# Optimization experiments

Hardware: AMD Instinct MI355X
Metric: run time of the kernel (lower is better)

The kernel has to match this reference:

```python
import jax, jax.numpy as jnp
import numpy as np

B, C_IN, C_OUT, H, W = 8, 512, 512, 64, 64
KS = 3
STYLE_DIM = 512
UP = 2            # AliasFreeConv passes upsample*2 = 2 to the activation
DOWN = 2
TAPS = 12
MARGIN = 10
NEG_SLOPE = 0.2
LRELU_SCALE = float(np.sqrt(2.0))  # fused_leaky_relu default scale
EPS = 1e-8


def _lowpass(taps):
    # 1D windowed-sinc lowpass (separable FIR), normalized to sum 1
    n = np.arange(taps)
    x = n - (taps - 1) / 2.0
    h = np.sinc(x / 2.0) * np.hanning(taps)
    return (h / h.sum()).astype(np.float32)


def upfirdn2d(x, kernel, up, down, pad):
    # x: (N,C,H,W); kernel: (kh,kw); up=(ux,uy); down=(dx,dy); pad=(px0,px1,py0,py1)
    # Semantics match rosinality upfirdn2d_native: zero-stuff, pad, convolve with
    # flipped kernel, stride-downsample. lhs_dilation gives (L-1)*u+1 samples, the
    # torch version keeps L*u (u-1 trailing zeros), so add u-1 to trailing pad.
    ux, uy = up
    dx, dy = down
    px0, px1, py0, py1 = pad
    N, C, H_, W_ = x.shape
    k = jnp.flip(kernel, axis=(0, 1))[None, None].astype(x.dtype)  # (1,1,kh,kw)
    y = x.reshape(N * C, 1, H_, W_)
    y = jax.lax.conv_general_dilated(
        y, k, window_strides=(dy, dx),
        padding=((py0, py1 + uy - 1), (px0, px1 + ux - 1)),
        lhs_dilation=(uy, ux),
        dimension_numbers=('NCHW', 'OIHW', 'NCHW'))
    return y.reshape(N, C, y.shape[2], y.shape[3])


def setup_inputs() -> dict:
    key = jax.random.key(0)
    ks = jax.random.split(key, 6)
    x = jax.random.normal(ks[0], (B, C_IN, H, W), jnp.float32)
    style = jax.random.normal(ks[1], (B, STYLE_DIM), jnp.float32)
    mod_w = jax.random.normal(ks[2], (C_IN, STYLE_DIM), jnp.float32)   # EqualLinear weight
    mod_b = jnp.ones((C_IN,), jnp.float32)                              # bias_init=1
    conv_w = jax.random.normal(ks[3], (C_OUT, C_IN, KS, KS), jnp.float32)
    act_b = jax.random.normal(ks[4], (C_OUT,), jnp.float32) * 0.1
    lp = jnp.asarray(_lowpass(TAPS))
    return {"x": x, "style": style, "mod_w": mod_w, "mod_b": mod_b,
            "conv_w": conv_w, "act_b": act_b, "up_filter": lp, "down_filter": lp}


def reference(x, style, mod_w, mod_b, conv_w, act_b, up_filter, down_filter):
    Bn, Cin, _, _ = x.shape
    # --- ModulatedConv2d (padding=False, eval mode: ema_var = 1) ---
    lin_scale = 1.0 / np.sqrt(STYLE_DIM)          # EqualLinear scale, lr_mul=1
    s = style @ (mod_w * lin_scale).T + mod_b     # (B, Cin)
    wscale = 1.0 / np.sqrt(Cin * KS * KS)
    w = wscale * conv_w[None] * s[:, None, :, None, None]  # (B, Cout, Cin, kh, kw)
    demod = jax.lax.rsqrt(jnp.sum(w * w, axis=(2, 3, 4)) + EPS)
    w = w * demod[:, :, None, None, None]
    w = w / (1.0 + EPS)                           # / (sqrt(ema_var)+eps), ema_var=1

    def conv_one(xi, wi):  # per-sample grouped conv (groups=batch), VALID padding
        return jax.lax.conv_general_dilated(
            xi[None], wi, (1, 1), 'VALID',
            dimension_numbers=('NCHW', 'OIHW', 'NCHW'))[0]
    out = jax.vmap(conv_one)(x, w)                # (B, Cout, H-2, W-2)

    # --- AliasFreeActivation ---
    out = out + act_b[None, :, None, None]
    fu = up_filter * UP                           # 1D filter scaled by upsample at init
    p = TAPS - UP
    up_pad = ((p + 1) // 2 + UP * 2 - 1, p // 2 + UP)  # padding flag False (ks==3)
    out = upfirdn2d(out, fu[None, :], up=(UP, 1), down=(1, 1),
                    pad=(up_pad[0], up_pad[1], 0, 0))
    out = upfirdn2d(out, fu[:, None], up=(1, UP), down=(1, 1),
                    pad=(0, 0, up_pad[0], up_pad[1]))
    out = jnp.where(out >= 0, out, NEG_SLOPE * out) * LRELU_SCALE
    p = TAPS - DOWN
    dpad = ((p + 1) // 2, p // 2)
    out = upfirdn2d(out, down_filter[None, :], up=(1, 1), down=(DOWN, 1),
                    pad=(dpad[0], dpad[1], 0, 0))
    out = upfirdn2d(out, down_filter[:, None], up=(1, 1), down=(1, DOWN),
                    pad=(0, 0, dpad[0], dpad[1]))
    m = (MARGIN * UP - MARGIN * DOWN) // 2        # = 0 here (static)
    if m > 0:
        out = out[:, :, m:-m, m:-m]
    return out
```

## Files before the change

### kernel.cpp

```cpp
#include <hip/hip_runtime.h>

typedef __attribute__((ext_vector_type(8))) short s16x8;
typedef __attribute__((ext_vector_type(4))) float f32x4;

__device__ __forceinline__ float b2f(unsigned short u){
  union { unsigned int i; float f; } v; v.i = ((unsigned int)u) << 16; return v.f;
}
__device__ __forceinline__ unsigned short f2b(float f){
  union { float f; unsigned int i; } v; v.f = f;
  unsigned int x = v.i;
  return (unsigned short)((x + 0x7fffu + ((x >> 16) & 1u)) >> 16);
}

__device__ __forceinline__ void ld_lds16(const unsigned short* g, unsigned short* l){
  __builtin_amdgcn_global_load_lds(
      (const __attribute__((address_space(1))) void*)g,
      (__attribute__((address_space(3))) void*)l, 16, 0, 0);
}

template<int BF16> struct In;
template<> struct In<1>{
  static __device__ __forceinline__ float ld(const void* p, size_t i){
    return b2f(((const unsigned short*)p)[i]);
  }
};
template<> struct In<0>{
  static __device__ __forceinline__ float ld(const void* p, size_t i){
    return ((const float*)p)[i];
  }
};

__global__ void k_detect(const unsigned int* __restrict__ mod_b, int* __restrict__ flag){
  *flag = (*mod_b == 0x3F803F80u) ? 1 : 0;
}

template<int BF16>
__device__ __forceinline__ void small_body(const void* actb, const void* upf, const void* dnf,
                                           float* actb_f, float* fu_f, float* fd_f){
  int t = threadIdx.x;
  actb_f[t] = In<BF16>::ld(actb, t);
  if(t < 12){
    fu_f[t] = 2.0f * In<BF16>::ld(upf, t);
    fd_f[t] = In<BF16>::ld(dnf, t);
  }
}
__global__ void k_small(const void* __restrict__ actb, const void* __restrict__ upf,
                        const void* __restrict__ dnf, float* __restrict__ actb_f,
                        float* __restrict__ fu_f, float* __restrict__ fd_f,
                        const int* __restrict__ flag){
  if(*flag) small_body<1>(actb, upf, dnf, actb_f, fu_f, fd_f);
  else      small_body<0>(actb, upf, dnf, actb_f, fu_f, fd_f);
}

template<int BF16>
__device__ __forceinline__ void style_body(const void* style, const void* mod_w,
                                           const void* mod_b, float* s){
  int gw = (blockIdx.x*256 + threadIdx.x) >> 6;
  int lane = threadIdx.x & 63;
  int b = gw >> 9, i = gw & 511;
  size_t so = (size_t)b*512 + lane*8;
  size_t mo = (size_t)i*512 + lane*8;
  float acc = 0.f;
  #pragma unroll
  for(int q=0;q<8;q++) acc += In<BF16>::ld(style, so+q)*In<BF16>::ld(mod_w, mo+q);
  #pragma unroll
  for(int m=32;m>=1;m>>=1) acc += __shfl_xor(acc, m, 64);
  if(lane == 0) s[gw] = acc * 0.044194173824159216f + In<BF16>::ld(mod_b, i);
}
__global__ __launch_bounds__(256) void k_style(
    const void* __restrict__ style, const void* __restrict__ mod_w,
    const void* __restrict__ mod_b, float* __restrict__ s,
    const int* __restrict__ flag){
  if(*flag) style_body<1>(style, mod_w, mod_b, s);
  else      style_body<0>(style, mod_w, mod_b, s);
}

template<int BF16>
__device__ __forceinline__ void wrepq_body(const void* conv_w, unsigned short* wrep2, float* wsq){
  int idx = blockIdx.x*256 + threadIdx.x;
  float v[9], acc = 0.f;
  #pragma unroll
  for(int t=0;t<9;t++){ v[t] = In<BF16>::ld(conv_w, (size_t)idx*9 + t); acc += v[t]*v[t]; }
  wsq[idx] = acc;
  #pragma unroll
  for(int t=0;t<9;t++) wrep2[t*262144 + idx] = f2b(v[t]);
}
__global__ __launch_bounds__(256) void k_wrepq(
    const void* __restrict__ conv_w, unsigned short* __restrict__ wrep2,
    float* __restrict__ wsq, const int* __restrict__ flag){
  if(*flag) wrepq_body<1>(conv_w, wrep2, wsq);
  else      wrepq_body<0>(conv_w, wrep2, wsq);
}

__global__ __launch_bounds__(256) void k_demod(
    const float* __restrict__ s, const float* __restrict__ wsq,
    float* __restrict__ rowscale){
  int gw = (blockIdx.x*256 + threadIdx.x) >> 6;
  int lane = threadIdx.x & 63;
  int b = gw >> 9, o = gw & 511;
  const float* sr = s + b*512 + lane*8;
  const float* wr = wsq + (size_t)o*512 + lane*8;
  float acc = 0.f;
  #pragma unroll
  for(int q=0;q<8;q++){ float sv = sr[q]; acc += sv*sv*wr[q]; }
  #pragma unroll
  for(int m=32;m>=1;m>>=1) acc += __shfl_xor(acc, m, 64);
  if(lane == 0){
    float demod = rsqrtf(acc*(1.0f/4608.0f) + 1e-8f);
    rowscale[gw] = 0.014731391274719742f * demod * (1.0f/(1.0f+1e-8f));
  }
}

template<int BF16>
__device__ __forceinline__ void xs_body(const void* x, const float* s,
                                        unsigned short* xs2, unsigned short* tl){
  int bh = blockIdx.x >> 3;
  int i0 = (blockIdx.x & 7) << 6;
  int b = bh >> 6, h = bh & 63;
  #pragma unroll
  for(int l=0;l<2;l++){
    int e = (threadIdx.x + l*256) << 3;
    int row = e >> 6, col = e & 63;
    size_t base = (((size_t)(b*512 + i0 + row))*64 + h)*64 + col;
    float sc = s[b*512 + i0 + row];
    alignas(16) unsigned short tmp[8];
    if(BF16){
      uint4 v = *(const uint4*)((const unsigned short*)x + base);
      const unsigned short* pv = (const unsigned short*)&v;
      #pragma unroll
      for(int q2=0;q2<8;q2++) tmp[q2] = f2b(b2f(pv[q2]) * sc);
    } else {
      float4 v0 = *(const float4*)((const float*)x + base);
      float4 v1 = *(const float4*)((const float*)x + base + 4);
      tmp[0]=f2b(v0.x*sc); tmp[1]=f2b(v0.y*sc); tmp[2]=f2b(v0.z*sc); tmp[3]=f2b(v0.w*sc);
      tmp[4]=f2b(v1.x*sc); tmp[5]=f2b(v1.y*sc); tmp[6]=f2b(v1.z*sc); tmp[7]=f2b(v1.w*sc);
    }
    *(uint4*)(tl + row*72 + col) = *(const uint4*)tmp;
  }
  __syncthreads();
  #pragma unroll
  for(int l=0;l<2;l++){
    int e = (threadIdx.x + l*256) << 3;
    int w = e >> 6, ic = e & 63;
    alignas(16) unsigned short tmp[8];
    #pragma unroll
    for(int q2=0;q2<8;q2++) tmp[q2] = tl[(ic + q2)*72 + w];
    *(uint4*)(xs2 + (((size_t)(b*64 + h))*64 + w)*512 + i0 + ic) = *(const uint4*)tmp;
  }
}
__global__ __launch_bounds__(256) void k_xs(
    const void* __restrict__ x, const float* __restrict__ s,
    unsigned short* __restrict__ xs2, const int* __restrict__ flag){
  __shared__ unsigned short tl[64*72];
  if(*flag) xs_body<1>(x, s, xs2, tl);
  else      xs_body<0>(x, s, xs2, tl);
}


#define MFMA16(a,b,c) __builtin_amdgcn_mfma_f32_16x16x32_bf16((a),(b),(c),0,0,0)
#define KBARRIER __builtin_amdgcn_s_barrier()
#define LGKM0 asm volatile("s_waitcnt lgkmcnt(0)" ::: "memory")
#define LGKM8 asm volatile("s_waitcnt lgkmcnt(8)" ::: "memory")
#define VMW4  asm volatile("s_waitcnt vmcnt(4)" ::: "memory")
#define VMW8  asm volatile("s_waitcnt vmcnt(8)" ::: "memory")
#define VMW0  asm volatile("s_waitcnt vmcnt(0)" ::: "memory")

template<int MH,int NH>
__device__ __forceinline__ void mmq(f32x4 (&acc)[8][4], const s16x8 (&Ax)[8], const s16x8 (&Bx)[4]){
  #pragma unroll
  for(int j=0;j<4;j++)
    #pragma unroll
    for(int k=0;k<2;k++){
      f32x4 c = acc[MH*4+j][NH*2+k];
      c = MFMA16(Ax[j*2+0], Bx[k*2+0], c);
      c = MFMA16(Ax[j*2+1], Bx[k*2+1], c);
      acc[MH*4+j][NH*2+k] = c;
    }
}

template<int BUF,int MH>
__device__ __forceinline__ void lda(s16x8 (&dst)[8], const unsigned short* lds,
                                    int arow, int c0, int c1){
  #pragma unroll
  for(int j=0;j<4;j++){
    const unsigned short* p = lds + BUF*32768 + arow + (MH*64 + j*16)*64;
    dst[j*2+0] = *(const s16x8*)(p + c0);
    dst[j*2+1] = *(const s16x8*)(p + c1);
  }
}

template<int BUF,int NH>
__device__ __forceinline__ void ldb(s16x8 (&dst)[4], const unsigned short* lds,
                                    int brow, int c0, int c1){
  #pragma unroll
  for(int k=0;k<2;k++){
    const unsigned short* p = lds + BUF*32768 + brow + (NH*2 + k)*16*64;
    dst[k*2+0] = *(const s16x8*)(p + c0);
    dst[k*2+1] = *(const s16x8*)(p + c1);
  }
}

template<int BUF,int H>
__device__ __forceinline__ void stga(const unsigned short* wrep2, unsigned short* lds,
                                     const unsigned (&aoff)[2][2], int sdst, int kt){
  unsigned koff = (unsigned)(kt >> 3)*262144u + (unsigned)(kt & 7)*64u;
  ld_lds16(wrep2 + aoff[H][0] + koff, lds + BUF*32768 + H*8192 + 0*4096 + sdst);
  ld_lds16(wrep2 + aoff[H][1] + koff, lds + BUF*32768 + H*8192 + 1*4096 + sdst);
}

template<int BUF,int H>
__device__ __forceinline__ void stgb(const unsigned short* xs2, unsigned short* lds,
                                     const unsigned (&boff)[2][2], int sdst, int kt){
  int t = kt >> 3;
  int kh = (t*11) >> 5;
  unsigned koff = (unsigned)(kh*64 + (t - kh*3))*512u + (unsigned)(kt & 7)*64u;
  ld_lds16(xs2 + boff[H][0] + koff, lds + BUF*32768 + 16384 + H*8192 + 0*4096 + sdst);
  ld_lds16(xs2 + boff[H][1] + koff, lds + BUF*32768 + 16384 + H*8192 + 1*4096 + sdst);
}

__global__ __launch_bounds__(512, 2) void k_conv(
    const unsigned short* __restrict__ wrep2,
    const unsigned short* __restrict__ xs2,
    const float* __restrict__ rowscale,
    const float* __restrict__ actb_f,
    unsigned short* __restrict__ out0){
  __shared__ unsigned short lds[65536];

  const int tid  = threadIdx.x;
  const int lane = tid & 63, wid = tid >> 6;
  const int wm = wid >> 2, wn = wid & 3;
  const int quad = lane >> 4, l16 = lane & 15, sw = l16 & 7;

  int w = blockIdx.x;
  int wsw = (w & 7)*31 + (w >> 3);
  const int mt = wsw & 1, nt = wsw >> 1;
  const int o0 = mt*256, p0 = nt*256;

  const int srow  = tid >> 3;
  const int sgoff = ((tid & 7) ^ (srow & 7)) * 8;
  unsigned aoff[2][2], boff[2][2];
  #pragma unroll
  for(int h=0;h<2;h++){
    #pragma unroll
    for(int r=0;r<2;r++){
      int row = srow + r*64 + h*128;
      aoff[h][r] = (unsigned)(o0 + row)*512u + (unsigned)sgoff;
      int p  = p0 + row;
      int bb = ((p >> 7)*529) >> 14;
      boff[h][r] = (unsigned)(p + bb*128)*512u + (unsigned)sgoff;
    }
  }
  const int sdst = wid*512;

  const int c0 = ((0*4 + quad) ^ sw) * 8;
  const int c1 = ((1*4 + quad) ^ sw) * 8;
  const int arow = (wm*128 + l16) * 64;
  const int brow = (wn*64  + l16) * 64 + 16384;

  f32x4 acc[8][4];
  f32x4 z = {0.f,0.f,0.f,0.f};
  #pragma unroll
  for(int a=0;a<8;a++)
    #pragma unroll
    for(int n=0;n<4;n++) acc[a][n] = z;

  s16x8 Aa[8], Ab[8], Ba[4], Bb[4];

  stga<0,0>(wrep2, lds, aoff, sdst, 0);
  stga<0,1>(wrep2, lds, aoff, sdst, 0);
  stgb<0,0>(xs2,   lds, boff, sdst, 0);
  stgb<0,1>(xs2,   lds, boff, sdst, 0);
  stga<1,0>(wrep2, lds, aoff, sdst, 1);
  stga<1,1>(wrep2, lds, aoff, sdst, 1);
  stgb<1,0>(xs2,   lds, boff, sdst, 1);
  stgb<1,1>(xs2,   lds, boff, sdst, 1);
  VMW8;
  KBARRIER;
  lda<0,0>(Aa, lds, arow, c0, c1);
  ldb<0,0>(Ba, lds, brow, c0, c1);

  #pragma unroll 1
  for(int it=0; it<36; ++it){
    const int T0 = 2*it;
    const int full = (it < 35);
    KBARRIER;
    ldb<0,1>(Bb, lds, brow, c0, c1);
    __builtin_amdgcn_s_setprio(1); mmq<0,0>(acc, Aa, Ba); __builtin_amdgcn_s_setprio(0);
    KBARRIER;
    lda<0,1>(Ab, lds, arow, c0, c1);
    __builtin_amdgcn_s_setprio(1); mmq<0,1>(acc, Aa, Bb); __builtin_amdgcn_s_setprio(0);
    LGKM8;
    KBARRIER;
    if(full){ stgb<0,0>(xs2, lds, boff, sdst, T0+2); stgb<0,1>(xs2, lds, boff, sdst, T0+2); }
    __builtin_amdgcn_s_setprio(1); mmq<1,0>(acc, Ab, Ba); __builtin_amdgcn_s_setprio(0);
    LGKM0;
    if(full){ VMW4; } else { VMW0; }
    KBARRIER;
    if(full){ stga<0,0>(wrep2, lds, aoff, sdst, T0+2); stga<0,1>(wrep2, lds, aoff, sdst, T0+2); }
    lda<1,0>(Aa, lds, arow, c0, c1);
    ldb<1,0>(Ba, lds, brow, c0, c1);
    __builtin_amdgcn_s_setprio(1); mmq<1,1>(acc, Ab, Bb); __builtin_amdgcn_s_setprio(0);
    KBARRIER;
    ldb<1,1>(Bb, lds, brow, c0, c1);
    __builtin_amdgcn_s_setprio(1); mmq<0,0>(acc, Aa, Ba); __builtin_amdgcn_s_setprio(0);
    KBARRIER;
    lda<1,1>(Ab, lds, arow, c0, c1);
    __builtin_amdgcn_s_setprio(1); mmq<0,1>(acc, Aa, Bb); __builtin_amdgcn_s_setprio(0);
    LGKM8;
    KBARRIER;
    if(full){ stgb<1,0>(xs2, lds, boff, sdst, T0+3); stgb<1,1>(xs2, lds, boff, sdst, T0+3); }
    __builtin_amdgcn_s_setprio(1); mmq<1,0>(acc, Ab, Ba); __builtin_amdgcn_s_setprio(0);
    LGKM0;
    if(full){ VMW4; }
    KBARRIER;
    if(full){
      stga<1,0>(wrep2, lds, aoff, sdst, T0+3);
      stga<1,1>(wrep2, lds, aoff, sdst, T0+3);
      lda<0,0>(Aa, lds, arow, c0, c1);
      ldb<0,0>(Ba, lds, brow, c0, c1);
    }
    __builtin_amdgcn_s_setprio(1); mmq<1,1>(acc, Ab, Bb); __builtin_amdgcn_s_setprio(0);
  }

  #pragma unroll
  for(int n=0;n<4;n++){
    int p  = p0 + wn*64 + n*16 + l16;
    int bn = ((p >> 7)*529) >> 14;
    int rem = p - bn*3968;
    const size_t obase = (size_t)bn*2031616u + (size_t)rem;
    const int rsb = bn*512;
    #pragma unroll
    for(int a=0;a<8;a++){
      int o = o0 + wm*128 + a*16 + quad*4;
      #pragma unroll
      for(int r=0;r<4;r++){
        float v = acc[a][n][r]*rowscale[rsb + o + r] + actb_f[o + r];
        out0[obase + (size_t)(o + r)*3968u] = f2b(v);
      }
    }
  }
}

__global__ __launch_bounds__(256) void k_filter(
    const unsigned short* __restrict__ out0,
    const float* __restrict__ fu_f,
    const float* __restrict__ fd_f,
    void* __restrict__ out,
    const int* __restrict__ flag){
  __shared__ unsigned short uvs[128*140];
  __shared__ unsigned short bufB[70*128];
  unsigned short* a0s = uvs;
  int bf = *flag;
  int bc = blockIdx.x;
  int tid = threadIdx.x;

  float fur[12], fdr[12];
  #pragma unroll
  for(int j=0;j<12;j++){ fur[j] = fu_f[j]; fdr[j] = fd_f[j]; }

  const uint4 z4 = {0,0,0,0};
  const unsigned short* src = out0 + (size_t)bc*62*64;
  for(int v=tid; v<496; v+=256)
    *(uint4*)(a0s + v*8) = *(const uint4*)(src + v*8);
  for(int idx=tid; idx<128; idx+=256){
    int r = idx >> 4, seg = idx & 15;
    *(uint4*)(bufB + ((r < 4) ? r : (r + 62))*128 + seg*8) = z4;
  }
  __syncthreads();

  for(int idx=tid; idx<62*16; idx+=256){
    int r = idx >> 4, tt0 = (idx & 15) << 2;
    const unsigned short* ar = a0s + r*64;
    float w[10];
    #pragma unroll
    for(int c=0;c<10;c++){
      int col = tt0 - 4 + c;
      w[c] = (col >= 0 && col < 62) ? b2f(ar[col]) : 0.f;
    }
    alignas(16) unsigned short tmp[8];
    #pragma unroll
    for(int u=0;u<4;u++){
      float accE = 0.f, accO = 0.f;
      #pragma unroll
      for(int jj=0;jj<6;jj++){
        accE += fur[2*jj+1]*w[u+5-jj];
        accO += fur[2*jj  ]*w[u+6-jj];
      }
      tmp[2*u]   = f2b(accE);
      tmp[2*u+1] = f2b(accO);
    }
    *(uint4*)(bufB + (r+4)*128 + 2*tt0) = *(const uint4*)tmp;
  }
  __syncthreads();

  for(int idx=tid; idx<16*128; idx+=256){
    int tr0 = (idx >> 7) << 2, o = idx & 127;
    float w[10];
    #pragma unroll
    for(int c=0;c<10;c++) w[c] = b2f(bufB[(tr0+c)*128 + o]);
    #pragma unroll
    for(int u=0;u<4;u++){
      float accE = 0.f, accO = 0.f;
      #pragma unroll
      for(int jj=0;jj<6;jj++){
        accE += fur[2*jj+1]*w[u+5-jj];
        accO += fur[2*jj  ]*w[u+6-jj];
      }
      accE = (accE >= 0.f ? accE : 0.2f*accE)*1.4142135623730951f;
      accO = (accO >= 0.f ? accO : 0.2f*accO)*1.4142135623730951f;
      int m = 2*(tr0+u);
      uvs[m*140 + 5 + o]     = f2b(accE);
      uvs[(m+1)*140 + 5 + o] = f2b(accO);
    }
  }
  for(int idx=tid; idx<1536; idx+=256){
    int m = (idx*2731) >> 15;
    int c = idx - m*12;
    uvs[m*140 + ((c < 5) ? c : (c + 128))] = 0;
  }
  __syncthreads();

  for(int idx=tid; idx<96; idx+=256){
    int r = idx >> 3, seg = idx & 7;
    *(uint4*)(bufB + ((r < 6) ? r : (r + 128))*64 + seg*8) = z4;
  }
  for(int idx=tid; idx<128*16; idx+=256){
    int m = idx >> 4, X0 = (idx & 15) << 2;
    const unsigned short* ur = uvs + m*140 + 2*X0;
    alignas(8) unsigned short wv[20];
    #pragma unroll
    for(int h=0;h<5;h++) *(uint2*)(wv + h*4) = *(const uint2*)(ur + h*4);
    alignas(8) unsigned short tmp[4];
    #pragma unroll
    for(int u=0;u<4;u++){
      float acc = 0.f;
      #pragma unroll
      for(int j=0;j<12;j++) acc += fdr[j]*b2f(wv[2*u+11-j]);
      tmp[u] = f2b(acc);
    }
    *(uint2*)(bufB + (m+6)*64 + X0) = *(const uint2*)tmp;
  }
  __syncthreads();

  for(int idx=tid; idx<16*64; idx+=256){
    int Y0 = (idx >> 6) << 2, X = idx & 63;
    float w[18];
    #pragma unroll
    for(int c=0;c<18;c++) w[c] = b2f(bufB[(2*Y0+1+c)*64 + X]);
    #pragma unroll
    for(int u=0;u<4;u++){
      float acc = 0.f;
      #pragma unroll
      for(int j=0;j<12;j++) acc += fdr[j]*w[2*u+11-j];
      if(bf) ((unsigned short*)out)[(size_t)bc*4096 + (Y0+u)*64 + X] = f2b(acc);
      else   ((float*)out)[(size_t)bc*4096 + (Y0+u)*64 + X] = acc;
    }
  }
}

extern "C" void kernel_launch(void* const* d_in, const int* in_sizes, int n_in,
                              void* d_out, int out_size, void* d_ws, size_t ws_size,
                              hipStream_t stream){
  const void* x     = d_in[0];
  const void* style = d_in[1];
  const void* mod_w = d_in[2];
  const void* mod_b = d_in[3];
  const void* convw = d_in[4];
  const void* actb  = d_in[5];
  const void* upf   = d_in[6];
  const void* dnf   = d_in[7];
  char* ws = (char*)d_ws;
  int*   flag   = (int*)(ws + 0);
  float* actb_f = (float*)(ws + 1024);
  float* fu_f   = (float*)(ws + 4096);
  float* fd_f   = (float*)(ws + 4224);
  float* s_buf  = (float*)(ws + 8192);
  float* rsc    = (float*)(ws + 24576);
  float* wsq    = (float*)(ws + 40960);
  unsigned short* wrep2 = (unsigned short*)(ws + 1089536);
  unsigned short* xs2   = (unsigned short*)(ws + 5808128);
  unsigned short* out0  = (unsigned short*)(ws + 39370752);
  if(ws_size < 71876608) return;

  k_detect<<<1, 1, 0, stream>>>((const unsigned int*)mod_b, flag);
  k_small<<<1, 512, 0, stream>>>(actb, upf, dnf, actb_f, fu_f, fd_f, flag);
  k_style<<<1024, 256, 0, stream>>>(style, mod_w, mod_b, s_buf, flag);
  k_wrepq<<<1024, 256, 0, stream>>>(convw, wrep2, wsq, flag);
  k_demod<<<1024, 256, 0, stream>>>(s_buf, wsq, rsc);
  k_xs<<<4096, 256, 0, stream>>>(x, s_buf, xs2, flag);
  k_conv<<<248, 512, 0, stream>>>(wrep2, xs2, rsc, actb_f, out0);
  k_filter<<<4096, 256, 0, stream>>>(out0, fu_f, fd_f, d_out, flag);
}
```

Measured before the change: 347.4 us.

## Switch conv GEMM inner loop from 16x16x32 to 32x32x16 bf16 MFMA

Replaces the 16x16x32 MFMA tiles with 32x32x16 bf16 MFMA in the implicit-GEMM conv main loop. Fragment loads, the LDS read swizzle, the accumulator layout (4x2 f32x16) and the epilogue row mapping all change to match. The larger MFMA shape is meant to cut LDS reads per FLOP and instruction-issue overhead. The waits change from lgkmcnt(8) to lgkmcnt(0), which removes some overlap of LDS loads with compute, and the new epilogue mapping adds a correctness risk.

```diff
diff --git a/kernel.cpp b/kernel.cpp
--- a/kernel.cpp
+++ b/kernel.cpp
@@ -2,6 +2,7 @@
 
 typedef __attribute__((ext_vector_type(8))) short s16x8;
 typedef __attribute__((ext_vector_type(4))) float f32x4;
+typedef __attribute__((ext_vector_type(16))) float f32x16;
 
 __device__ __forceinline__ float b2f(unsigned short u){
   union { unsigned int i; float f; } v; v.i = ((unsigned int)u) << 16; return v.f;
@@ -157,47 +158,42 @@
 }
 
 
-#define MFMA16(a,b,c) __builtin_amdgcn_mfma_f32_16x16x32_bf16((a),(b),(c),0,0,0)
+#define MFMA32(a,b,c) __builtin_amdgcn_mfma_f32_32x32x16_bf16((a),(b),(c),0,0,0)
 #define KBARRIER __builtin_amdgcn_s_barrier()
 #define LGKM0 asm volatile("s_waitcnt lgkmcnt(0)" ::: "memory")
-#define LGKM8 asm volatile("s_waitcnt lgkmcnt(8)" ::: "memory")
 #define VMW4  asm volatile("s_waitcnt vmcnt(4)" ::: "memory")
 #define VMW8  asm volatile("s_waitcnt vmcnt(8)" ::: "memory")
 #define VMW0  asm volatile("s_waitcnt vmcnt(0)" ::: "memory")
 
-template<int MH,int NH>
-__device__ __forceinline__ void mmq(f32x4 (&acc)[8][4], const s16x8 (&Ax)[8], const s16x8 (&Bx)[4]){
-  #pragma unroll
-  for(int j=0;j<4;j++)
-    #pragma unroll
-    for(int k=0;k<2;k++){
-      f32x4 c = acc[MH*4+j][NH*2+k];
-      c = MFMA16(Ax[j*2+0], Bx[k*2+0], c);
-      c = MFMA16(Ax[j*2+1], Bx[k*2+1], c);
-      acc[MH*4+j][NH*2+k] = c;
-    }
-}
-
-template<int BUF,int MH>
-__device__ __forceinline__ void lda(s16x8 (&dst)[8], const unsigned short* lds,
-                                    int arow, int c0, int c1){
-  #pragma unroll
-  for(int j=0;j<4;j++){
-    const unsigned short* p = lds + BUF*32768 + arow + (MH*64 + j*16)*64;
-    dst[j*2+0] = *(const s16x8*)(p + c0);
-    dst[j*2+1] = *(const s16x8*)(p + c1);
-  }
-}
-
-template<int BUF,int NH>
-__device__ __forceinline__ void ldb(s16x8 (&dst)[4], const unsigned short* lds,
-                                    int brow, int c0, int c1){
-  #pragma unroll
-  for(int k=0;k<2;k++){
-    const unsigned short* p = lds + BUF*32768 + brow + (NH*2 + k)*16*64;
-    dst[k*2+0] = *(const s16x8*)(p + c0);
-    dst[k*2+1] = *(const s16x8*)(p + c1);
-  }
+template<int BUF,int MH,int KH>
+__device__ __forceinline__ void ldA32(s16x8 (&d)[4], const unsigned short* lds,
+                                      int abase, const int (&ck)[4]){
+  #pragma unroll
+  for(int mt2=0;mt2<2;mt2++)
+    #pragma unroll
+    for(int ks2=0;ks2<2;ks2++)
+      d[mt2*2+ks2] = *(const s16x8*)(lds + BUF*32768 + abase + (MH*2+mt2)*2048 + ck[KH*2+ks2]);
+}
+template<int BUF,int KH>
+__device__ __forceinline__ void ldB32(s16x8 (&d)[4], const unsigned short* lds,
+                                      int bbase, const int (&ck)[4]){
+  #pragma unroll
+  for(int nt2=0;nt2<2;nt2++)
+    #pragma unroll
+    for(int ks2=0;ks2<2;ks2++)
+      d[nt2*2+ks2] = *(const s16x8*)(lds + BUF*32768 + 16384 + bbase + nt2*2048 + ck[KH*2+ks2]);
+}
+template<int MH>
+__device__ __forceinline__ void mma32(f32x16 (&acc)[4][2], const s16x8 (&A)[4], const s16x8 (&B)[4]){
+  #pragma unroll
+  for(int mt2=0;mt2<2;mt2++)
+    #pragma unroll
+    for(int nt2=0;nt2<2;nt2++){
+      f32x16 c = acc[MH*2+mt2][nt2];
+      c = MFMA32(A[mt2*2+0], B[nt2*2+0], c);
+      c = MFMA32(A[mt2*2+1], B[nt2*2+1], c);
+      acc[MH*2+mt2][nt2] = c;
+    }
 }
 
 template<int BUF,int H>
@@ -229,7 +225,7 @@
   const int tid  = threadIdx.x;
   const int lane = tid & 63, wid = tid >> 6;
   const int wm = wid >> 2, wn = wid & 3;
-  const int quad = lane >> 4, l16 = lane & 15, sw = l16 & 7;
+  const int r5 = lane & 31, hi = lane >> 5, l7 = lane & 7;
 
   int w = blockIdx.x;
   int wsw = (w & 7)*31 + (w >> 3);
@@ -252,19 +248,21 @@
   }
   const int sdst = wid*512;
 
-  const int c0 = ((0*4 + quad) ^ sw) * 8;
-  const int c1 = ((1*4 + quad) ^ sw) * 8;
-  const int arow = (wm*128 + l16) * 64;
-  const int brow = (wn*64  + l16) * 64 + 16384;
-
-  f32x4 acc[8][4];
-  f32x4 z = {0.f,0.f,0.f,0.f};
-  #pragma unroll
-  for(int a=0;a<8;a++)
-    #pragma unroll
-    for(int n=0;n<4;n++) acc[a][n] = z;
-
-  s16x8 Aa[8], Ab[8], Ba[4], Bb[4];
+  const int abase = (wm*128 + r5)*64;
+  const int bbase = (wn*64  + r5)*64;
+  int ck[4];
+  #pragma unroll
+  for(int ks=0;ks<4;ks++) ck[ks] = ((ks*2 + hi) ^ l7) * 8;
+
+  f32x16 acc[4][2];
+  #pragma unroll
+  for(int a=0;a<4;a++)
+    #pragma unroll
+    for(int n=0;n<2;n++)
+      #pragma unroll
+      for(int e=0;e<16;e++) acc[a][n][e] = 0.f;
+
+  s16x8 Aa[4], Ab[4], Aa2[4], Ab2[4], Bc[4], Bd[4];
 
   stga<0,0>(wrep2, lds, aoff, sdst, 0);
   stga<0,1>(wrep2, lds, aoff, sdst, 0);
@@ -276,66 +274,71 @@
   stgb<1,1>(xs2,   lds, boff, sdst, 1);
   VMW8;
   KBARRIER;
-  lda<0,0>(Aa, lds, arow, c0, c1);
-  ldb<0,0>(Ba, lds, brow, c0, c1);
+  ldA32<0,0,0>(Aa, lds, abase, ck);
+  ldB32<0,0>(Bc, lds, bbase, ck);
 
   #pragma unroll 1
   for(int it=0; it<36; ++it){
     const int T0 = 2*it;
     const int full = (it < 35);
     KBARRIER;
-    ldb<0,1>(Bb, lds, brow, c0, c1);
-    __builtin_amdgcn_s_setprio(1); mmq<0,0>(acc, Aa, Ba); __builtin_amdgcn_s_setprio(0);
-    KBARRIER;
-    lda<0,1>(Ab, lds, arow, c0, c1);
-    __builtin_amdgcn_s_setprio(1); mmq<0,1>(acc, Aa, Bb); __builtin_amdgcn_s_setprio(0);
-    LGKM8;
+    ldA32<0,1,0>(Ab, lds, abase, ck);
+    __builtin_amdgcn_s_setprio(1); mma32<0>(acc, Aa, Bc); __builtin_amdgcn_s_setprio(0);
+    KBARRIER;
+    ldA32<0,0,1>(Aa2, lds, abase, ck);
+    ldB32<0,1>(Bd, lds, bbase, ck);
+    __builtin_amdgcn_s_setprio(1); mma32<1>(acc, Ab, Bc); __builtin_amdgcn_s_setprio(0);
+    LGKM0;
     KBARRIER;
     if(full){ stgb<0,0>(xs2, lds, boff, sdst, T0+2); stgb<0,1>(xs2, lds, boff, sdst, T0+2); }
-    __builtin_amdgcn_s_setprio(1); mmq<1,0>(acc, Ab, Ba); __builtin_amdgcn_s_setprio(0);
+    ldA32<0,1,1>(Ab2, lds, abase, ck);
+    __builtin_amdgcn_s_setprio(1); mma32<0>(acc, Aa2, Bd); __builtin_amdgcn_s_setprio(0);
     LGKM0;
     if(full){ VMW4; } else { VMW0; }
     KBARRIER;
     if(full){ stga<0,0>(wrep2, lds, aoff, sdst, T0+2); stga<0,1>(wrep2, lds, aoff, sdst, T0+2); }
-    lda<1,0>(Aa, lds, arow, c0, c1);
-    ldb<1,0>(Ba, lds, brow, c0, c1);
-    __builtin_amdgcn_s_setprio(1); mmq<1,1>(acc, Ab, Bb); __builtin_amdgcn_s_setprio(0);
-    KBARRIER;
-    ldb<1,1>(Bb, lds, brow, c0, c1);
-    __builtin_amdgcn_s_setprio(1); mmq<0,0>(acc, Aa, Ba); __builtin_amdgcn_s_setprio(0);
-    KBARRIER;
-    lda<1,1>(Ab, lds, arow, c0, c1);
-    __builtin_amdgcn_s_setprio(1); mmq<0,1>(acc, Aa, Bb); __builtin_amdgcn_s_setprio(0);
-    LGKM8;
+    ldA32<1,0,0>(Aa, lds, abase, ck);
+    ldB32<1,0>(Bc, lds, bbase, ck);
+    __builtin_amdgcn_s_setprio(1); mma32<1>(acc, Ab2, Bd); __builtin_amdgcn_s_setprio(0);
+    KBARRIER;
+    ldA32<1,1,0>(Ab, lds, abase, ck);
+    __builtin_amdgcn_s_setprio(1); mma32<0>(acc, Aa, Bc); __builtin_amdgcn_s_setprio(0);
+    KBARRIER;
+    ldA32<1,0,1>(Aa2, lds, abase, ck);
+    ldB32<1,1>(Bd, lds, bbase, ck);
+    __builtin_amdgcn_s_setprio(1); mma32<1>(acc, Ab, Bc); __builtin_amdgcn_s_setprio(0);
+    LGKM0;
     KBARRIER;
     if(full){ stgb<1,0>(xs2, lds, boff, sdst, T0+3); stgb<1,1>(xs2, lds, boff, sdst, T0+3); }
-    __builtin_amdgcn_s_setprio(1); mmq<1,0>(acc, Ab, Ba); __builtin_amdgcn_s_setprio(0);
+    ldA32<1,1,1>(Ab2, lds, abase, ck);
+    __builtin_amdgcn_s_setprio(1); mma32<0>(acc, Aa2, Bd); __builtin_amdgcn_s_setprio(0);
     LGKM0;
     if(full){ VMW4; }
     KBARRIER;
     if(full){
       stga<1,0>(wrep2, lds, aoff, sdst, T0+3);
       stga<1,1>(wrep2, lds, aoff, sdst, T0+3);
-      lda<0,0>(Aa, lds, arow, c0, c1);
-      ldb<0,0>(Ba, lds, brow, c0, c1);
-    }
-    __builtin_amdgcn_s_setprio(1); mmq<1,1>(acc, Ab, Bb); __builtin_amdgcn_s_setprio(0);
-  }
-
-  #pragma unroll
-  for(int n=0;n<4;n++){
-    int p  = p0 + wn*64 + n*16 + l16;
+      ldA32<0,0,0>(Aa, lds, abase, ck);
+      ldB32<0,0>(Bc, lds, bbase, ck);
+    }
+    __builtin_amdgcn_s_setprio(1); mma32<1>(acc, Ab2, Bd); __builtin_amdgcn_s_setprio(0);
+  }
+
+  #pragma unroll
+  for(int n2=0;n2<2;n2++){
+    int p  = p0 + wn*64 + n2*32 + r5;
     int bn = ((p >> 7)*529) >> 14;
     int rem = p - bn*3968;
     const size_t obase = (size_t)bn*2031616u + (size_t)rem;
     const int rsb = bn*512;
     #pragma unroll
-    for(int a=0;a<8;a++){
-      int o = o0 + wm*128 + a*16 + quad*4;
-      #pragma unroll
-      for(int r=0;r<4;r++){
-        float v = acc[a][n][r]*rowscale[rsb + o + r] + actb_f[o + r];
-        out0[obase + (size_t)(o + r)*3968u] = f2b(v);
+    for(int a=0;a<4;a++){
+      #pragma unroll
+      for(int reg=0;reg<16;reg++){
+        int ro = (reg & 3) + 8*(reg >> 2) + 4*hi;
+        int o = o0 + wm*128 + a*32 + ro;
+        float v = acc[a][n2][reg]*rowscale[rsb + o] + actb_f[o];
+        out0[obase + (size_t)o*3968u] = f2b(v);
       }
     }
   }
```

Measured after the change: 377.7 us. +8.7%, slower.
